# Optimization experiments

Measured on AMD Instinct MI355X. Metric: run time of the kernel, lower is better.

The kernel has to match this reference:

```python
import jax, jax.numpy as jnp
import numpy as np

H = 16  # n_heads

def setup_inputs() -> dict:
    key = jax.random.key(0)
    k1, k2, k3, k4 = jax.random.split(key, 4)
    B, S, D = 2, 2048, 1024
    query = jax.random.normal(k1, (B, S, D), dtype=jnp.float32)
    pos_emb = jax.random.normal(k2, (S, D), dtype=jnp.float32)
    w_qkv = jax.random.normal(k3, (D, 3 * D), dtype=jnp.float32) * (D ** -0.5)
    w_out = jax.random.normal(k4, (D, D), dtype=jnp.float32) * (D ** -0.5)
    return {"query": query, "pos_emb": pos_emb, "w_qkv": w_qkv, "w_out": w_out}

def reference(query, pos_emb, w_qkv, w_out):
    B, S, D = query.shape
    d_k = D // H
    # ape=True: pos_fn applied to input before QKV projection (additive APE)
    x = query + pos_emb[None, :, :]
    # fused QKV projection; torch view(B,S,H,3*d_k) + chunk(3,-1) == reshape(B,S,H,3,d_k)
    qkv = jnp.einsum('bsd,de->bse', x, w_qkv).reshape(B, S, H, 3, d_k)
    qkv = jnp.transpose(qkv, (0, 2, 1, 3, 4))  # [B,H,S,3,d_k]
    q, k, v = qkv[..., 0, :], qkv[..., 1, :], qkv[..., 2, :]
    scale = d_k ** -0.5
    scores = jnp.einsum('bhqd,bhkd->bhqk', q, k) * scale  # [B,H,S,S]
    attn = jax.nn.softmax(scores, axis=-1)  # dropout is identity in eval
    o = jnp.einsum('bhqk,bhkd->bhqd', attn, v)
    o = jnp.transpose(o, (0, 2, 1, 3)).reshape(B, S, D)
    return jnp.einsum('bsd,de->bse', o, w_out)
```

## Files before the change

### kernel.cpp

```cpp
#include <hip/hip_runtime.h>

#define SS 2048
#define DD 1024
#define N3 3072

typedef unsigned short u16;
typedef unsigned int u32;
typedef __attribute__((ext_vector_type(8))) short bf16x8;
typedef __attribute__((ext_vector_type(4))) float f32x4;

__device__ __forceinline__ u16 f2bf(float f) {
    u32 u = __float_as_uint(f);
    u32 r = u + 0x7fffu + ((u >> 16) & 1u);
    return (u16)(r >> 16);
}

__device__ __forceinline__ float fast_exp2(float x) {
    return __builtin_amdgcn_exp2f(x);
}

__device__ __forceinline__ void async_cp16(u16* lds, const u16* g) {
    __builtin_amdgcn_global_load_lds((const __attribute__((address_space(1))) u32*)g,
                                     (__attribute__((address_space(3))) u32*)lds, 16, 0, 0);
}

__global__ __launch_bounds__(256)
void prep_x(const float* __restrict__ q, const float* __restrict__ pos, u16* __restrict__ x)
{
    const size_t i = ((size_t)blockIdx.x * 256 + threadIdx.x) * 4;
    float4 a = *(const float4*)(q + i);
    float4 p = *(const float4*)(pos + (i & (size_t)(SS * DD - 1)));
    uint2 r;
    r.x = (u32)f2bf(a.x + p.x) | ((u32)f2bf(a.y + p.y) << 16);
    r.y = (u32)f2bf(a.z + p.z) | ((u32)f2bf(a.w + p.w) << 16);
    *(uint2*)(x + i) = r;
}

__global__ __launch_bounds__(256)
void transpose_bf16(const float* __restrict__ W, u16* __restrict__ WT, int K, int N)
{
    __shared__ float t[32][33];
    const int tx = threadIdx.x & 31, ty = threadIdx.x >> 5;
    const int x0 = blockIdx.x * 32, y0 = blockIdx.y * 32;
#pragma unroll
    for (int i = 0; i < 4; ++i)
        t[ty + i * 8][tx] = W[(size_t)(y0 + ty + i * 8) * N + x0 + tx];
    __syncthreads();
#pragma unroll
    for (int i = 0; i < 4; ++i)
        WT[(size_t)(x0 + ty + i * 8) * K + y0 + tx] = f2bf(t[tx][ty + i * 8]);
}

template <int OUT_BF16, int NT>
__global__ __launch_bounds__(256)
void gemm_mfma(const u16* __restrict__ A, const u16* __restrict__ BT,
               void* __restrict__ Cv, int M, int N, int K)
{
    constexpr int FR = NT / 32;
    __shared__ u16 As[128 * 32];
    __shared__ u16 Bs[NT * 32];

    const int tid = threadIdx.x;
    const int lane = tid & 63, wv = tid >> 6;
    const int quad = lane >> 4, l16 = lane & 15;
    const int m0 = blockIdx.y * 128, n0 = blockIdx.x * NT;

    const int srow = wv * 32 + (lane >> 2);
    const int scol = (lane & 3) * 8;
    const u16* ag = A + (size_t)(m0 + srow) * K + scol;
    u16* al = As + srow * 32 + scol;

    const u16* bg;
    u16* bl;
    if constexpr (NT == 128) {
        bg = BT + (size_t)(n0 + srow) * K + scol;
        bl = Bs + srow * 32 + scol;
    } else {
        const int srB = tid >> 2, scB = (tid & 3) * 8;
        bg = BT + (size_t)(n0 + srB) * K + scB;
        bl = Bs + srB * 32 + scB;
    }

    const int moff = (wv >> 1) * 64, noff = (wv & 1) * (NT / 2);

    f32x4 acc[4][FR];
#pragma unroll
    for (int i = 0; i < 4; ++i)
#pragma unroll
        for (int j = 0; j < FR; ++j) acc[i][j] = {0.f, 0.f, 0.f, 0.f};

    for (int k0 = 0; k0 < K; k0 += 32) {
        async_cp16(al, ag + k0);
        async_cp16(al + 16 * 32, ag + k0 + (size_t)16 * K);
        async_cp16(bl, bg + k0);
        if constexpr (NT == 128)
            async_cp16(bl + 16 * 32, bg + k0 + (size_t)16 * K);
        __syncthreads();

        bf16x8 af[4], bfr[FR];
#pragma unroll
        for (int t = 0; t < 4; ++t)
            af[t]  = *(const bf16x8*)&As[(moff + t * 16 + l16) * 32 + quad * 8];
#pragma unroll
        for (int t = 0; t < FR; ++t)
            bfr[t] = *(const bf16x8*)&Bs[(noff + t * 16 + l16) * 32 + quad * 8];
#pragma unroll
        for (int mt = 0; mt < 4; ++mt)
#pragma unroll
            for (int nt = 0; nt < FR; ++nt)
                acc[mt][nt] = __builtin_amdgcn_mfma_f32_16x16x32_bf16(af[mt], bfr[nt], acc[mt][nt], 0, 0, 0);
        __syncthreads();
    }

#pragma unroll
    for (int mt = 0; mt < 4; ++mt)
#pragma unroll
        for (int r = 0; r < 4; ++r) {
            const size_t row = m0 + moff + mt * 16 + quad * 4 + r;
            if (OUT_BF16) {
                u16* cp = (u16*)Cv + row * N + n0 + noff + l16;
#pragma unroll
                for (int nt = 0; nt < FR; ++nt) cp[nt * 16] = f2bf(acc[mt][nt][r]);
            } else {
                float* cp = (float*)Cv + row * N + n0 + noff + l16;
#pragma unroll
                for (int nt = 0; nt < FR; ++nt) cp[nt * 16] = acc[mt][nt][r];
            }
        }
}

__global__ __launch_bounds__(256)
void attn_mfma(const u16* __restrict__ qkv, u16* __restrict__ o)
{
    __shared__ u16 Ks[64 * 64];
    __shared__ u16 Vn[64 * 64];
    __shared__ u16 Vt[64 * 64];
    __shared__ u16 Ps[4][32 * 64];

    const int tid = threadIdx.x;
    const int lane = tid & 63, wv = tid >> 6;
    const int quad = lane >> 4, l16 = lane & 15;
    const int qt = blockIdx.x, h = blockIdx.y, b = blockIdx.z;

    const size_t hb = (size_t)b * SS * N3 + h * 192;
    const int q0 = qt * 128 + wv * 32;
    const int sw = l16 & 7;

    bf16x8 qf[2][2];
#pragma unroll
    for (int mt = 0; mt < 2; ++mt)
#pragma unroll
        for (int ks = 0; ks < 2; ++ks)
            qf[mt][ks] = *(const bf16x8*)(qkv + hb + (size_t)(q0 + mt * 16 + l16) * N3 + ks * 32 + quad * 8);

    f32x4 po[2][4];
#pragma unroll
    for (int mt = 0; mt < 2; ++mt)
#pragma unroll
        for (int nt = 0; nt < 4; ++nt) po[mt][nt] = {0.f, 0.f, 0.f, 0.f};
    float lrun[2] = {0.f, 0.f};

    const int skey = tid >> 2;
    const int sc16 = (tid & 3) * 16;
    const int c0 = (tid & 3) * 2;
    const u16* kg = qkv + hb + 64 + (size_t)skey * N3 + sc16;
    const u16* vg = kg + 64;
    const int ksw = skey & 7;
    u16* kst0 = &Ks[skey * 64 + (((c0    ) ^ ksw) << 3)];
    u16* kst1 = &Ks[skey * 64 + (((c0 + 1) ^ ksw) << 3)];
    u16* vst0 = &Vn[skey * 64 + (((c0    ) ^ ksw) << 3)];
    u16* vst1 = &Vn[skey * 64 + (((c0 + 1) ^ ksw) << 3)];

    const int kp = tid & 31, dkb = (tid >> 5) * 8;

    const float CEXP = 0.125f * 1.44269504f;

    for (int kt = 0; kt < SS / 64; ++kt) {
        const size_t koff = (size_t)kt * 64 * N3;
        uint4 kv0 = *(const uint4*)(kg + koff);
        uint4 kv1 = *(const uint4*)(kg + koff + 8);
        uint4 vv0 = *(const uint4*)(vg + koff);
        uint4 vv1 = *(const uint4*)(vg + koff + 8);
        *(uint4*)kst0 = kv0;  *(uint4*)kst1 = kv1;
        *(uint4*)vst0 = vv0;  *(uint4*)vst1 = vv1;
        __syncthreads();

        {
            uint4 a4 = *(const uint4*)&Vn[(2 * kp)     * 64 + (((dkb >> 3) ^ ((2 * kp)     & 7)) << 3)];
            uint4 b4 = *(const uint4*)&Vn[(2 * kp + 1) * 64 + (((dkb >> 3) ^ ((2 * kp + 1) & 7)) << 3)];
            u32 ar[4] = {a4.x, a4.y, a4.z, a4.w};
            u32 br[4] = {b4.x, b4.y, b4.z, b4.w};
#pragma unroll
            for (int j = 0; j < 8; ++j) {
                const u32 sel = (j & 1) ? 0x07060302u : 0x05040100u;
                const u32 w = __builtin_amdgcn_perm(br[j >> 1], ar[j >> 1], sel);
                const int row = dkb + j;
                *(u32*)&Vt[row * 64 + (((kp >> 2) ^ (row & 7)) << 3) + ((2 * kp) & 7)] = w;
            }
        }

        f32x4 sf[2][4];
#pragma unroll
        for (int mt = 0; mt < 2; ++mt)
#pragma unroll
            for (int kn = 0; kn < 4; ++kn) sf[mt][kn] = {0.f, 0.f, 0.f, 0.f};
#pragma unroll
        for (int ks = 0; ks < 2; ++ks)
#pragma unroll
            for (int kn = 0; kn < 4; ++kn) {
                bf16x8 kf = *(const bf16x8*)&Ks[(kn * 16 + l16) * 64 + (((ks * 4 + quad) ^ sw) << 3)];
#pragma unroll
                for (int mt = 0; mt < 2; ++mt)
                    sf[mt][kn] = __builtin_amdgcn_mfma_f32_16x16x32_bf16(kf, qf[mt][ks], sf[mt][kn], 0, 0, 0);
            }

#pragma unroll
        for (int mt = 0; mt < 2; ++mt) {
            float ls = 0.f;
#pragma unroll
            for (int kn = 0; kn < 4; ++kn) {
                const float p0 = fast_exp2(sf[mt][kn][0] * CEXP);
                const float p1 = fast_exp2(sf[mt][kn][1] * CEXP);
                const float p2 = fast_exp2(sf[mt][kn][2] * CEXP);
                const float p3 = fast_exp2(sf[mt][kn][3] * CEXP);
                const u32 w0 = __builtin_amdgcn_perm(__float_as_uint(p1), __float_as_uint(p0), 0x07060302u);
                const u32 w1 = __builtin_amdgcn_perm(__float_as_uint(p3), __float_as_uint(p2), 0x07060302u);
                ls += __uint_as_float(w0 << 16) + __uint_as_float(w0 & 0xffff0000u)
                    + __uint_as_float(w1 << 16) + __uint_as_float(w1 & 0xffff0000u);
                const int ch = (2 * kn + (quad >> 1)) ^ sw;
                uint2 wp; wp.x = w0; wp.y = w1;
                *(uint2*)&Ps[wv][(mt * 16 + l16) * 64 + (ch << 3) + ((quad & 1) << 2)] = wp;
            }
            lrun[mt] += ls;
        }
        __syncthreads();

#pragma unroll
        for (int ks = 0; ks < 2; ++ks) {
            bf16x8 pf[2], vf[4];
#pragma unroll
            for (int mt = 0; mt < 2; ++mt)
                pf[mt] = *(const bf16x8*)&Ps[wv][(mt * 16 + l16) * 64 + (((ks * 4 + quad) ^ sw) << 3)];
#pragma unroll
            for (int nt = 0; nt < 4; ++nt)
                vf[nt] = *(const bf16x8*)&Vt[(nt * 16 + l16) * 64 + (((ks * 4 + quad) ^ sw) << 3)];
#pragma unroll
            for (int mt = 0; mt < 2; ++mt)
#pragma unroll
                for (int nt = 0; nt < 4; ++nt)
                    po[mt][nt] = __builtin_amdgcn_mfma_f32_16x16x32_bf16(pf[mt], vf[nt], po[mt][nt], 0, 0, 0);
        }
        __syncthreads();
    }

#pragma unroll
    for (int mt = 0; mt < 2; ++mt) {
        lrun[mt] += __shfl_xor(lrun[mt], 16, 64);
        lrun[mt] += __shfl_xor(lrun[mt], 32, 64);
    }
#pragma unroll
    for (int mt = 0; mt < 2; ++mt) {
        float linv[4];
#pragma unroll
        for (int r = 0; r < 4; ++r)
            linv[r] = 1.f / __shfl(lrun[mt], quad * 4 + r, 64);
#pragma unroll
        for (int r = 0; r < 4; ++r) {
            const size_t row = (size_t)b * SS + q0 + mt * 16 + quad * 4 + r;
            u16* op = o + row * DD + h * 64 + l16;
#pragma unroll
            for (int nt = 0; nt < 4; ++nt)
                op[nt * 16] = f2bf(po[mt][nt][r] * linv[r]);
        }
    }
}

extern "C" void kernel_launch(void* const* d_in, const int* in_sizes, int n_in,
                              void* d_out, int out_size, void* d_ws, size_t ws_size,
                              hipStream_t stream)
{
    const float* query  = (const float*)d_in[0];
    const float* posemb = (const float*)d_in[1];
    const float* w_qkv  = (const float*)d_in[2];
    const float* w_out  = (const float*)d_in[3];
    float* out = (float*)d_out;

    u16* xb    = (u16*)d_ws;
    u16* wqkvT = xb    + (size_t)4096 * 1024;
    u16* woutT = wqkvT + (size_t)3072 * 1024;
    u16* qkv   = woutT + (size_t)1024 * 1024;
    u16* ob    = qkv   + (size_t)4096 * 3072;

    prep_x<<<4096, 256, 0, stream>>>(query, posemb, xb);
    transpose_bf16<<<dim3(N3 / 32, DD / 32), 256, 0, stream>>>(w_qkv, wqkvT, DD, N3);
    transpose_bf16<<<dim3(DD / 32, DD / 32), 256, 0, stream>>>(w_out, woutT, DD, DD);

    gemm_mfma<1, 128><<<dim3(N3 / 128, 4096 / 128), 256, 0, stream>>>(xb, wqkvT, (void*)qkv, 4096, N3, DD);

    attn_mfma<<<dim3(SS / 128, 16, 2), 256, 0, stream>>>(qkv, ob);

    gemm_mfma<0, 64><<<dim3(DD / 64, 4096 / 128), 256, 0, stream>>>(ob, woutT, (void*)out, 4096, DD, DD);
}
```

Measured before the change: 213.5 us.

## Fuse positional add and bf16 cast into QKV GEMM A-load; flatten attention grid

Removes the separate prep_x kernel. The new QKV GEMM loads fp32 query and pos_emb directly, adds them, converts to bf16 and writes the result to LDS, so the intermediate bf16 x buffer is never written or re-read. The cost is that each A tile is now loaded as fp32 through synchronous register loads (twice the bytes) instead of async LDS copies, and that work is repeated across all 24 N-blocks. The attention launch also becomes a 1D grid with heads and batch innermost, which changes block scheduling order.

```diff
diff --git a/kernel.cpp b/kernel.cpp
--- a/kernel.cpp
+++ b/kernel.cpp
@@ -15,6 +15,10 @@
     return (u16)(r >> 16);
 }
 
+__device__ __forceinline__ u32 pack2bf(float x, float y) {
+    return (u32)f2bf(x) | ((u32)f2bf(y) << 16);
+}
+
 __device__ __forceinline__ float fast_exp2(float x) {
     return __builtin_amdgcn_exp2f(x);
 }
@@ -25,18 +29,6 @@
 }
 
 __global__ __launch_bounds__(256)
-void prep_x(const float* __restrict__ q, const float* __restrict__ pos, u16* __restrict__ x)
-{
-    const size_t i = ((size_t)blockIdx.x * 256 + threadIdx.x) * 4;
-    float4 a = *(const float4*)(q + i);
-    float4 p = *(const float4*)(pos + (i & (size_t)(SS * DD - 1)));
-    uint2 r;
-    r.x = (u32)f2bf(a.x + p.x) | ((u32)f2bf(a.y + p.y) << 16);
-    r.y = (u32)f2bf(a.z + p.z) | ((u32)f2bf(a.w + p.w) << 16);
-    *(uint2*)(x + i) = r;
-}
-
-__global__ __launch_bounds__(256)
 void transpose_bf16(const float* __restrict__ W, u16* __restrict__ WT, int K, int N)
 {
     __shared__ float t[32][33];
@@ -49,6 +41,80 @@
 #pragma unroll
     for (int i = 0; i < 4; ++i)
         WT[(size_t)(x0 + ty + i * 8) * K + y0 + tx] = f2bf(t[tx][ty + i * 8]);
+}
+
+__global__ __launch_bounds__(256)
+void gemm_qkv(const float* __restrict__ Xf, const float* __restrict__ pos,
+              const u16* __restrict__ BT, u16* __restrict__ C)
+{
+    __shared__ u16 As[128 * 32];
+    __shared__ u16 Bs[128 * 32];
+
+    const int tid = threadIdx.x;
+    const int lane = tid & 63, wv = tid >> 6;
+    const int quad = lane >> 4, l16 = lane & 15;
+    const int m0 = blockIdx.y * 128, n0 = blockIdx.x * 128;
+
+    const int srow = wv * 32 + (lane >> 2);
+    const int scol = (lane & 3) * 8;
+
+    const float* q0p = Xf + (size_t)(m0 + srow) * DD + scol;
+    const float* p0p = pos + (size_t)((m0 + srow) & (SS - 1)) * DD + scol;
+    const u16* bg = BT + (size_t)(n0 + srow) * DD + scol;
+    u16* al = As + srow * 32 + scol;
+    u16* bl = Bs + srow * 32 + scol;
+
+    const int moff = (wv >> 1) * 64, noff = (wv & 1) * 64;
+
+    f32x4 acc[4][4];
+#pragma unroll
+    for (int i = 0; i < 4; ++i)
+#pragma unroll
+        for (int j = 0; j < 4; ++j) acc[i][j] = {0.f, 0.f, 0.f, 0.f};
+
+    for (int k0 = 0; k0 < DD; k0 += 32) {
+        async_cp16(bl, bg + k0);
+        async_cp16(bl + 16 * 32, bg + k0 + (size_t)16 * DD);
+#pragma unroll
+        for (int rr = 0; rr < 2; ++rr) {
+            const float* qp = q0p + k0 + (size_t)(rr * 16) * DD;
+            const float* pp = p0p + k0 + (size_t)(rr * 16) * DD;
+            float4 a0 = *(const float4*)qp;
+            float4 a1 = *(const float4*)(qp + 4);
+            float4 b0 = *(const float4*)pp;
+            float4 b1 = *(const float4*)(pp + 4);
+            uint4 w;
+            w.x = pack2bf(a0.x + b0.x, a0.y + b0.y);
+            w.y = pack2bf(a0.z + b0.z, a0.w + b0.w);
+            w.z = pack2bf(a1.x + b1.x, a1.y + b1.y);
+            w.w = pack2bf(a1.z + b1.z, a1.w + b1.w);
+            *(uint4*)(al + rr * 16 * 32) = w;
+        }
+        __syncthreads();
+
+        bf16x8 af[4], bfr[4];
+#pragma unroll
+        for (int t = 0; t < 4; ++t) {
+            af[t]  = *(const bf16x8*)&As[(moff + t * 16 + l16) * 32 + quad * 8];
+            bfr[t] = *(const bf16x8*)&Bs[(noff + t * 16 + l16) * 32 + quad * 8];
+        }
+#pragma unroll
+        for (int mt = 0; mt < 4; ++mt)
+#pragma unroll
+            for (int nt = 0; nt < 4; ++nt)
+                acc[mt][nt] = __builtin_amdgcn_mfma_f32_16x16x32_bf16(af[mt], bfr[nt], acc[mt][nt], 0, 0, 0);
+        __syncthreads();
+    }
+
+#pragma unroll
+    for (int mt = 0; mt < 4; ++mt)
+#pragma unroll
+        for (int r = 0; r < 4; ++r) {
+            const size_t row = m0 + moff + mt * 16 + quad * 4 + r;
+            u16* cp = C + row * N3 + n0 + noff + l16;
+#pragma unroll
+            for (int nt = 0; nt < 4; ++nt) cp[nt * 16] = f2bf(acc[mt][nt][r]);
+        }
 }
 
 template <int OUT_BF16, int NT>
@@ -140,7 +206,8 @@
     const int tid = threadIdx.x;
     const int lane = tid & 63, wv = tid >> 6;
     const int quad = lane >> 4, l16 = lane & 15;
-    const int qt = blockIdx.x, h = blockIdx.y, b = blockIdx.z;
+    const int bx = blockIdx.x;
+    const int h = bx & 15, b = (bx >> 4) & 1, qt = bx >> 5;
 
     const size_t hb = (size_t)b * SS * N3 + h * 192;
     const int q0 = qt * 128 + wv * 32;
@@ -285,19 +352,17 @@
     const float* w_out  = (const float*)d_in[3];
     float* out = (float*)d_out;
 
-    u16* xb    = (u16*)d_ws;
-    u16* wqkvT = xb    + (size_t)4096 * 1024;
+    u16* wqkvT = (u16*)d_ws;
     u16* woutT = wqkvT + (size_t)3072 * 1024;
     u16* qkv   = woutT + (size_t)1024 * 1024;
     u16* ob    = qkv   + (size_t)4096 * 3072;
 
-    prep_x<<<4096, 256, 0, stream>>>(query, posemb, xb);
     transpose_bf16<<<dim3(N3 / 32, DD / 32), 256, 0, stream>>>(w_qkv, wqkvT, DD, N3);
     transpose_bf16<<<dim3(DD / 32, DD / 32), 256, 0, stream>>>(w_out, woutT, DD, DD);
 
-    gemm_mfma<1, 128><<<dim3(N3 / 128, 4096 / 128), 256, 0, stream>>>(xb, wqkvT, (void*)qkv, 4096, N3, DD);
-
-    attn_mfma<<<dim3(SS / 128, 16, 2), 256, 0, stream>>>(qkv, ob);
+    gemm_qkv<<<dim3(N3 / 128, 4096 / 128), 256, 0, stream>>>(query, posemb, wqkvT, qkv);
+
+    attn_mfma<<<dim3(512, 1, 1), 256, 0, stream>>>(qkv, ob);
 
     gemm_mfma<0, 64><<<dim3(DD / 64, 4096 / 128), 256, 0, stream>>>(ob, woutT, (void*)out, 4096, DD, DD);
 }
```

New measurement: 235.1 us. 10.1% more time.

## Double GEMM K-tile to 64 with XOR-swizzled LDS and flatten attention grid

Applied to the files above, without the earlier changes.

The GEMM kernel now stages 64-wide K slices per iteration instead of 32, which halves the number of barrier pairs. It stores tiles in LDS with an XOR swizzle on 16-byte chunks to avoid bank conflicts on the fragment reads. The attention launch becomes a 1D grid of 512 blocks, with head and batch in the low bits, so consecutive blocks spread across heads and batches rather than query tiles. LDS use per GEMM block doubles, which may lower occupancy.

```diff
diff --git a/kernel.cpp b/kernel.cpp
--- a/kernel.cpp
+++ b/kernel.cpp
@@ -57,29 +57,24 @@
                void* __restrict__ Cv, int M, int N, int K)
 {
     constexpr int FR = NT / 32;
-    __shared__ u16 As[128 * 32];
-    __shared__ u16 Bs[NT * 32];
+    __shared__ u16 As[128 * 64];
+    __shared__ u16 Bs[NT * 64];
 
     const int tid = threadIdx.x;
     const int lane = tid & 63, wv = tid >> 6;
     const int quad = lane >> 4, l16 = lane & 15;
     const int m0 = blockIdx.y * 128, n0 = blockIdx.x * NT;
 
-    const int srow = wv * 32 + (lane >> 2);
-    const int scol = (lane & 3) * 8;
-    const u16* ag = A + (size_t)(m0 + srow) * K + scol;
-    u16* al = As + srow * 32 + scol;
-
-    const u16* bg;
-    u16* bl;
-    if constexpr (NT == 128) {
-        bg = BT + (size_t)(n0 + srow) * K + scol;
-        bl = Bs + srow * 32 + scol;
-    } else {
-        const int srB = tid >> 2, scB = (tid & 3) * 8;
-        bg = BT + (size_t)(n0 + srB) * K + scB;
-        bl = Bs + srB * 32 + scB;
-    }
+    const int arow = wv * 32 + (lane >> 3);
+    const int pc   = lane & 7;
+    const int lcA  = pc ^ (arow & 7);
+    const u16* agp = A + (size_t)(m0 + arow) * K + lcA * 8;
+    u16* alp = As + arow * 64 + pc * 8;
+
+    const int brow = (NT == 128) ? (wv * 32 + (lane >> 3)) : (wv * 8 + (lane >> 3));
+    const int lcB  = pc ^ (brow & 7);
+    const u16* bgp = BT + (size_t)(n0 + brow) * K + lcB * 8;
+    u16* blp = Bs + brow * 64 + pc * 8;
 
     const int moff = (wv >> 1) * 64, noff = (wv & 1) * (NT / 2);
 
@@ -89,26 +84,38 @@
 #pragma unroll
         for (int j = 0; j < FR; ++j) acc[i][j] = {0.f, 0.f, 0.f, 0.f};
 
-    for (int k0 = 0; k0 < K; k0 += 32) {
-        async_cp16(al, ag + k0);
-        async_cp16(al + 16 * 32, ag + k0 + (size_t)16 * K);
-        async_cp16(bl, bg + k0);
-        if constexpr (NT == 128)
-            async_cp16(bl + 16 * 32, bg + k0 + (size_t)16 * K);
-        __syncthreads();
-
-        bf16x8 af[4], bfr[FR];
-#pragma unroll
-        for (int t = 0; t < 4; ++t)
-            af[t]  = *(const bf16x8*)&As[(moff + t * 16 + l16) * 32 + quad * 8];
-#pragma unroll
-        for (int t = 0; t < FR; ++t)
-            bfr[t] = *(const bf16x8*)&Bs[(noff + t * 16 + l16) * 32 + quad * 8];
-#pragma unroll
-        for (int mt = 0; mt < 4; ++mt)
-#pragma unroll
-            for (int nt = 0; nt < FR; ++nt)
-                acc[mt][nt] = __builtin_amdgcn_mfma_f32_16x16x32_bf16(af[mt], bfr[nt], acc[mt][nt], 0, 0, 0);
+    const int swf = l16 & 7;
+
+    for (int k0 = 0; k0 < K; k0 += 64) {
+#pragma unroll
+        for (int s = 0; s < 4; ++s)
+            async_cp16(alp + s * 8 * 64, agp + (size_t)(s * 8) * K + k0);
+        if constexpr (NT == 128) {
+#pragma unroll
+            for (int s = 0; s < 4; ++s)
+                async_cp16(blp + s * 8 * 64, bgp + (size_t)(s * 8) * K + k0);
+        } else {
+#pragma unroll
+            for (int s = 0; s < 2; ++s)
+                async_cp16(blp + s * 32 * 64, bgp + (size_t)(s * 32) * K + k0);
+        }
+        __syncthreads();
+
+#pragma unroll
+        for (int ks = 0; ks < 2; ++ks) {
+            bf16x8 af[4], bfr[FR];
+#pragma unroll
+            for (int t = 0; t < 4; ++t)
+                af[t] = *(const bf16x8*)&As[(moff + t * 16 + l16) * 64 + (((ks * 4 + quad) ^ swf) << 3)];
+#pragma unroll
+            for (int t = 0; t < FR; ++t)
+                bfr[t] = *(const bf16x8*)&Bs[(noff + t * 16 + l16) * 64 + (((ks * 4 + quad) ^ swf) << 3)];
+#pragma unroll
+            for (int mt = 0; mt < 4; ++mt)
+#pragma unroll
+                for (int nt = 0; nt < FR; ++nt)
+                    acc[mt][nt] = __builtin_amdgcn_mfma_f32_16x16x32_bf16(af[mt], bfr[nt], acc[mt][nt], 0, 0, 0);
+        }
         __syncthreads();
     }
 
@@ -140,7 +147,8 @@
     const int tid = threadIdx.x;
     const int lane = tid & 63, wv = tid >> 6;
     const int quad = lane >> 4, l16 = lane & 15;
-    const int qt = blockIdx.x, h = blockIdx.y, b = blockIdx.z;
+    const int bx = blockIdx.x;
+    const int h = bx & 15, b = (bx >> 4) & 1, qt = bx >> 5;
 
     const size_t hb = (size_t)b * SS * N3 + h * 192;
     const int q0 = qt * 128 + wv * 32;
@@ -297,7 +305,7 @@
 
     gemm_mfma<1, 128><<<dim3(N3 / 128, 4096 / 128), 256, 0, stream>>>(xb, wqkvT, (void*)qkv, 4096, N3, DD);
 
-    attn_mfma<<<dim3(SS / 128, 16, 2), 256, 0, stream>>>(qkv, ob);
+    attn_mfma<<<dim3(512, 1, 1), 256, 0, stream>>>(qkv, ob);
 
     gemm_mfma<0, 64><<<dim3(DD / 64, 4096 / 128), 256, 0, stream>>>(ob, woutT, (void*)out, 4096, DD, DD);
 }
```

Result: faster. 204.6 us (-4.2%).
